# Performance work log

Hardware: AMD Instinct MI355X
Metric: run time of the kernel (lower is better)

Reference implementation:

```python
import jax, jax.numpy as jnp
import numpy as np

SCALE_BASE = 512.0
GAMMA = 0.96875


def _rotate_every_two(x):
    x1 = x[..., ::2]
    x2 = x[..., 1::2]
    return jnp.stack([-x2, x1], axis=-1).reshape(x.shape)


def _dup_interleave(m):
    # [L, d/2] -> [L, d], each column duplicated: (a,b) -> (a,a,b,b)
    return jnp.repeat(m, 2, axis=-1)


def _xpos(x, downscale=False):
    # x: [B, L, d]; offset = 0 (parallel form)
    B, L, d = x.shape
    half = d // 2
    pos = jnp.arange(L, dtype=x.dtype)
    # xpos per-channel scale base
    sv = (jnp.arange(0, d, 2, dtype=x.dtype) + 0.4 * d) / (1.4 * d)   # [d/2]
    scale = sv[None, :] ** (pos[:, None] / SCALE_BASE)                 # [L, d/2]
    if downscale:
        scale = 1.0 / scale
    inv_freq = 1.0 / (10000.0 ** (jnp.arange(half, dtype=x.dtype) / half))
    sinusoid = pos[:, None] * inv_freq[None, :]                        # [L, d/2]
    sin = _dup_interleave(jnp.sin(sinusoid) * scale)                   # [L, d]
    cos = _dup_interleave(jnp.cos(sinusoid) * scale)                   # [L, d]
    return x * cos[None] + _rotate_every_two(x) * sin[None]


def _get_D(seq_len, dtype):
    idx = jnp.arange(seq_len)
    diff = idx[:, None] - idx[None, :]                                 # n - m
    safe = jnp.where(diff >= 0, diff, 0).astype(dtype)
    return jnp.where(diff >= 0, GAMMA ** safe, jnp.zeros((), dtype))   # [L, L]


def setup_inputs() -> dict:
    key = jax.random.key(0)
    k1, k2, k3, k4 = jax.random.split(key, 4)
    B, L, H, D = 2, 4096, 1024, 64
    X = jax.random.normal(k1, (B, L, H), dtype=jnp.float32)
    W_Q = jax.random.normal(k2, (H, D), dtype=jnp.float32) / H
    W_K = jax.random.normal(k3, (H, D), dtype=jnp.float32) / H
    W_V = jax.random.normal(k4, (H, D), dtype=jnp.float32) / H
    return {"X": X, "W_Q": W_Q, "W_K": W_K, "W_V": W_V}


def reference(X, W_Q, W_K, W_V):
    L = X.shape[1]
    Dmask = _get_D(L, X.dtype)                     # [L, L]
    Q = _xpos(X @ W_Q)                             # [B, L, d]
    K = _xpos(X @ W_K, downscale=True)             # [B, L, d]
    V = X @ W_V                                    # [B, L, v]
    ret = jnp.einsum('bnd,bmd->bnm', Q, K) * Dmask[None]  # [B, L, L]
    return ret @ V                                 # [B, L, v]
```

## Files before the change

kernel.cpp:

```cpp
#include <hip/hip_runtime.h>
#include <math.h>

#define NB 2
#define LL 4096
#define HH 1024
#define DD 64
#define CHK 64
#define NCH 64
#define BLROWS (NB*LL)
#define NCHT (NB*NCH)
#define GAMMA 0.96875f

typedef _Float16 f16x8 __attribute__((ext_vector_type(8)));
typedef _Float16 f16x4 __attribute__((ext_vector_type(4)));
typedef float    f32x4 __attribute__((ext_vector_type(4)));

#define WCH 12288

__global__ __launch_bounds__(256) void prep_w(
    const float* __restrict__ WQ, const float* __restrict__ WK,
    const float* __restrict__ WV, _Float16* __restrict__ Whg,
    _Float16* __restrict__ Wlg)
{
    const unsigned t = blockIdx.x * 256 + threadIdx.x;
    const unsigned kchunk = t / 1536u;
    const unsigned s = t - kchunk * 1536u;
    const int ct2  = s >> 6;
    const int lane = s & 63;
    const int n16  = ct2 >> 1;
    const int kt   = ct2 & 1;
    const int quad = lane >> 4;
    const int n    = n16 * 16 + (lane & 15);
    const int k0   = (int)kchunk * 64 + kt * 32 + quad * 8;
    const int m    = n >> 6;
    const int d    = n & 63;
    const float* Wm = (m == 0) ? WQ : (m == 1) ? WK : WV;
    f16x8 hv, lv;
#pragma unroll
    for (int j = 0; j < 8; ++j) {
        const float x = Wm[(size_t)(k0 + j) * DD + d] * 1024.f;
        const _Float16 h = (_Float16)x;
        hv[j] = h;
        lv[j] = (_Float16)(x - (float)h);
    }
    *(f16x8*)&Whg[(size_t)t * 8] = hv;
    *(f16x8*)&Wlg[(size_t)t * 8] = lv;
}

__global__ __launch_bounds__(256) void proj_mfma(
    const float* __restrict__ X, const _Float16* __restrict__ Whg,
    const _Float16* __restrict__ Wlg, _Float16* __restrict__ Qr,
    _Float16* __restrict__ Kr, _Float16* __restrict__ Vr)
{
    __shared__ __align__(16) _Float16 lds[28672];
    _Float16* Xh = lds;
    _Float16* Xl = lds + 2048;
    _Float16* Wh = lds + 4096;
    _Float16* Wl = lds + 16384;

    const int tid  = threadIdx.x;
    const int wv   = tid >> 6;
    const int lane = tid & 63;
    const int r0   = blockIdx.x * 32;

    const int xrow = tid >> 3;
    const int xk8  = (tid & 7) * 8;
    const int xslot = (((xrow >> 4) * 2 + (xk8 >> 5)) * 64 +
                       ((xk8 >> 3) & 3) * 16 + (xrow & 15)) * 8;

    f32x4 acc[6];
#pragma unroll
    for (int i = 0; i < 6; ++i) acc[i] = (f32x4){0.f, 0.f, 0.f, 0.f};

    float4 pxa, pxb;
    f16x8  pwh[6], pwl[6];
    {
        const float* xp = &X[(size_t)(r0 + xrow) * HH + xk8];
        pxa = *(const float4*)&xp[0];
        pxb = *(const float4*)&xp[4];
#pragma unroll
        for (int i = 0; i < 6; ++i) {
            pwh[i] = *(const f16x8*)&Whg[(size_t)(tid + i * 256) * 8];
            pwl[i] = *(const f16x8*)&Wlg[(size_t)(tid + i * 256) * 8];
        }
    }

    for (int ch = 0; ch < 16; ++ch) {
        __syncthreads();
        {
            const float xv[8] = {pxa.x, pxa.y, pxa.z, pxa.w,
                                 pxb.x, pxb.y, pxb.z, pxb.w};
            f16x8 hv, lv;
#pragma unroll
            for (int e = 0; e < 8; ++e) {
                const _Float16 h = (_Float16)xv[e];
                hv[e] = h;
                lv[e] = (_Float16)(xv[e] - (float)h);
            }
            *(f16x8*)&Xh[xslot] = hv;
            *(f16x8*)&Xl[xslot] = lv;
#pragma unroll
            for (int i = 0; i < 6; ++i) {
                *(f16x8*)&Wh[(tid + i * 256) * 8] = pwh[i];
                *(f16x8*)&Wl[(tid + i * 256) * 8] = pwl[i];
            }
        }
        __syncthreads();
        if (ch + 1 < 16) {
            const float* xp = &X[(size_t)(r0 + xrow) * HH + (ch + 1) * 64 + xk8];
            pxa = *(const float4*)&xp[0];
            pxb = *(const float4*)&xp[4];
            const size_t cb = (size_t)(ch + 1) * WCH;
#pragma unroll
            for (int i = 0; i < 6; ++i) {
                pwh[i] = *(const f16x8*)&Whg[cb + (size_t)(tid + i * 256) * 8];
                pwl[i] = *(const f16x8*)&Wlg[cb + (size_t)(tid + i * 256) * 8];
            }
        }
#pragma unroll
        for (int kt = 0; kt < 2; ++kt) {
            const f16x8 a0h = *(const f16x8*)&Xh[((0 * 2 + kt) * 64 + lane) * 8];
            const f16x8 a0l = *(const f16x8*)&Xl[((0 * 2 + kt) * 64 + lane) * 8];
            const f16x8 a1h = *(const f16x8*)&Xh[((1 * 2 + kt) * 64 + lane) * 8];
            const f16x8 a1l = *(const f16x8*)&Xl[((1 * 2 + kt) * 64 + lane) * 8];
#pragma unroll
            for (int cj = 0; cj < 3; ++cj) {
                const int ctg = wv * 3 + cj;
                const f16x8 bh = *(const f16x8*)&Wh[((ctg * 2 + kt) * 64 + lane) * 8];
                const f16x8 bl = *(const f16x8*)&Wl[((ctg * 2 + kt) * 64 + lane) * 8];
                acc[cj] = __builtin_amdgcn_mfma_f32_16x16x32_f16(a0h, bh, acc[cj], 0, 0, 0);
                acc[cj] = __builtin_amdgcn_mfma_f32_16x16x32_f16(a0h, bl, acc[cj], 0, 0, 0);
                acc[cj] = __builtin_amdgcn_mfma_f32_16x16x32_f16(a0l, bh, acc[cj], 0, 0, 0);
                acc[3 + cj] = __builtin_amdgcn_mfma_f32_16x16x32_f16(a1h, bh, acc[3 + cj], 0, 0, 0);
                acc[3 + cj] = __builtin_amdgcn_mfma_f32_16x16x32_f16(a1h, bl, acc[3 + cj], 0, 0, 0);
                acc[3 + cj] = __builtin_amdgcn_mfma_f32_16x16x32_f16(a1l, bh, acc[3 + cj], 0, 0, 0);
            }
        }
    }

    const int quad = lane >> 4;
    const int c16  = lane & 15;
#pragma unroll
    for (int rt = 0; rt < 2; ++rt) {
#pragma unroll
        for (int cj = 0; cj < 3; ++cj) {
            const int ctg = wv * 3 + cj;
            const f32x4 v = acc[rt * 3 + cj];
            const int col = ctg * 16 + c16;
            const int mat = ctg >> 2;
            const int d   = col & 63;
            if (mat < 2) {
                const int i2 = d >> 1;
                const float sv   = (2.f * (float)i2 + 25.6f) / 89.6f;
                const float l2sv = log2f(sv);
                const float ifr  = exp2f(-13.28771237954945f * ((float)i2 / 32.f));
                const float sgn  = (mat == 0) ? 1.f : -1.f;
                _Float16* dst = (mat == 0) ? Qr : Kr;
#pragma unroll
                for (int r = 0; r < 4; ++r) {
                    const int row = r0 + rt * 16 + quad * 4 + r;
                    const float val = v[r] * (1.f / 1024.f);
                    const float p = __shfl_xor(val, 1, 64);
                    const float pf  = (float)(row & (LL - 1));
                    const float pfs = (float)(row & 63);
                    const float scl = exp2f(sgn * (pfs * (1.f / 512.f)) * l2sv);
                    float s, c;
                    sincosf(pf * ifr, &s, &c);
                    s *= scl; c *= scl;
                    const float o = ((col & 1) == 0) ? val * c - p * s
                                                     : val * c + p * s;
                    dst[(size_t)row * DD + d] = (_Float16)o;
                }
            } else {
#pragma unroll
                for (int r = 0; r < 4; ++r) {
                    const int row = r0 + rt * 16 + quad * 4 + r;
                    Vr[(size_t)row * DD + d] = (_Float16)(v[r] * (1.f / 1024.f));
                }
            }
        }
    }
}

__global__ __launch_bounds__(256) void chunk_kv(
    const _Float16* __restrict__ Kr, const _Float16* __restrict__ Vr,
    float* __restrict__ U)
{
    __shared__ _Float16 Kl[64 * 64];
    __shared__ _Float16 Vl[64 * 32];
    __shared__ float pwd[64];
    const int tid   = threadIdx.x;
    const int bc    = blockIdx.x;
    const int chunk = bc >> 1;
    const int dph   = (bc & 1) * 32;
    const size_t rbase = (size_t)chunk * CHK * DD;
    const float l2g = log2f(GAMMA);

    if (tid < 64) pwd[tid] = exp2f((float)(63 - tid) * l2g);
    {
        const int row = tid >> 2;
        const int c0  = (tid & 3) * 16;
        *(f16x8*)&Kl[row * 64 + c0]     = *(const f16x8*)&Kr[rbase + (size_t)row * DD + c0];
        *(f16x8*)&Kl[row * 64 + c0 + 8] = *(const f16x8*)&Kr[rbase + (size_t)row * DD + c0 + 8];
        const int c1 = (tid & 3) * 8;
        *(f16x8*)&Vl[row * 32 + c1] = *(const f16x8*)&Vr[rbase + (size_t)row * DD + dph + c1];
    }
    __syncthreads();
    const int dgr = tid >> 4;
    const int dc  = tid & 15;
    float a[4][2] = {{0,0},{0,0},{0,0},{0,0}};
#pragma unroll 8
    for (int j = 0; j < CHK; ++j) {
        const f16x4 kh = *(const f16x4*)&Kl[j * 64 + dgr * 4];
        const float w  = pwd[j];
        const float v0 = (float)Vl[j * 32 + dc * 2]     * w;
        const float v1 = (float)Vl[j * 32 + dc * 2 + 1] * w;
        const float k0 = (float)kh[0], k1 = (float)kh[1];
        const float k2 = (float)kh[2], k3 = (float)kh[3];
        a[0][0] += k0 * v0; a[0][1] += k0 * v1;
        a[1][0] += k1 * v0; a[1][1] += k1 * v1;
        a[2][0] += k2 * v0; a[2][1] += k2 * v1;
        a[3][0] += k3 * v0; a[3][1] += k3 * v1;
    }
#pragma unroll
    for (int r = 0; r < 4; ++r) {
        *(float2*)&U[((size_t)chunk * DD + dgr * 4 + r) * DD + dph + dc * 2] =
            make_float2(a[r][0], a[r][1]);
    }
}

__global__ __launch_bounds__(256) void prep_vt(
    const _Float16* __restrict__ Vr, const float* __restrict__ U,
    _Float16* __restrict__ VTf)
{
    __shared__ float    Tl[64 * 68];
    __shared__ _Float16 Vl[64 * 72];
    const int tid   = threadIdx.x;
    const int chunk = blockIdx.x;
    const int cloc  = chunk & 63;
    const size_t rbase = (size_t)chunk * CHK * DD;
    const float l2g = log2f(GAMMA);

    {
        const int row = tid >> 2;
        const int c0  = (tid & 3) * 16;
        *(f16x8*)&Vl[row * 72 + c0]     = *(const f16x8*)&Vr[rbase + (size_t)row * DD + c0];
        *(f16x8*)&Vl[row * 72 + c0 + 8] = *(const f16x8*)&Vr[rbase + (size_t)row * DD + c0 + 8];
    }
    {
        const int d  = tid >> 2;
        const int dq = (tid & 3) * 16;
        const float sv = (2.f * (float)(d >> 1) + 25.6f) / 89.6f;
        const float l2sv = log2f(sv);
        float acc[16];
#pragma unroll
        for (int i = 0; i < 16; ++i) acc[i] = 0.f;
        for (int dl = 1; dl <= 8; ++dl) {
            if (dl <= cloc) {
                const float f = exp2f(64.f * (float)(dl - 1) * l2g +
                                      0.125f * (float)dl * l2sv);
                const float* up = &U[((size_t)(chunk - dl) * DD + d) * DD + dq];
#pragma unroll
                for (int i4 = 0; i4 < 4; ++i4) {
                    const float4 u = *(const float4*)&up[i4 * 4];
                    acc[i4 * 4 + 0] += f * u.x; acc[i4 * 4 + 1] += f * u.y;
                    acc[i4 * 4 + 2] += f * u.z; acc[i4 * 4 + 3] += f * u.w;
                }
            }
        }
#pragma unroll
        for (int i = 0; i < 16; ++i) Tl[d * 68 + dq + i] = acc[i];
    }
    __syncthreads();
#pragma unroll
    for (int it = 0; it < 4; ++it) {
        const int s    = tid + it * 256;
        const int nt   = s >> 8;
        const int ks   = (s >> 6) & 3;
        const int lane = s & 63;
        const int quad = lane >> 4;
        const int dp   = nt * 16 + (lane & 15);
        const int mb   = ks * 32 + quad * 8;
        f16x8 v;
#pragma unroll
        for (int j = 0; j < 8; ++j) {
            const int mrow = mb + j;
            v[j] = (mrow < 64) ? Vl[mrow * 72 + dp]
                               : (_Float16)Tl[(mrow - 64) * 68 + dp];
        }
        *(f16x8*)&VTf[(size_t)chunk * 8192 + (size_t)s * 8] = v;
    }
}

__global__ __launch_bounds__(256) void chunk_out(
    const _Float16* __restrict__ Qr, const _Float16* __restrict__ Kr,
    const _Float16* __restrict__ VTf, float* __restrict__ out)
{
    __shared__ _Float16 Sb[32 * 136];
    __shared__ float pwl[65];
    const int tid   = threadIdx.x;
    const int bc    = blockIdx.x;
    const int chunk = bc >> 1;
    const int nh    = (bc & 1) * 32;
    const int w     = tid >> 6;
    const int lane  = tid & 63;
    const int quad  = lane >> 4;
    const int l15   = lane & 15;
    const int mtile = w >> 1;
    const int npair = (w & 1) * 2;
    const size_t rowbase = (size_t)chunk * CHK + nh;

    if (tid < 65) pwl[tid] = exp2f((float)tid * log2f(GAMMA));

    f16x8 aQ[2], bK[2][2];
#pragma unroll
    for (int ks = 0; ks < 2; ++ks)
        aQ[ks] = *(const f16x8*)&Qr[(rowbase + mtile * 16 + l15) * DD +
                                    ks * 32 + quad * 8];
#pragma unroll
    for (int nt = 0; nt < 2; ++nt)
#pragma unroll
        for (int ks = 0; ks < 2; ++ks)
            bK[nt][ks] = *(const f16x8*)&Kr[((size_t)chunk * CHK +
                                            (npair + nt) * 16 + l15) * DD +
                                            ks * 32 + quad * 8];
    __syncthreads();

    f32x4 sA[2] = {(f32x4){0.f,0.f,0.f,0.f}, (f32x4){0.f,0.f,0.f,0.f}};
#pragma unroll
    for (int nt = 0; nt < 2; ++nt)
#pragma unroll
        for (int ks = 0; ks < 2; ++ks)
            sA[nt] = __builtin_amdgcn_mfma_f32_16x16x32_f16(aQ[ks], bK[nt][ks],
                                                            sA[nt], 0, 0, 0);
#pragma unroll
    for (int nt = 0; nt < 2; ++nt) {
        const int m = (npair + nt) * 16 + l15;
#pragma unroll
        for (int r = 0; r < 4; ++r) {
            const int nl = mtile * 16 + quad * 4 + r;
            const int n64 = nh + nl;
            const float val = (n64 >= m) ? sA[nt][r] * pwl[n64 - m] : 0.f;
            Sb[nl * 136 + m] = (_Float16)val;
        }
    }
    if ((w & 1) == 0) {
        const float g = pwl[nh + mtile * 16 + l15 + 1];
#pragma unroll
        for (int ks = 0; ks < 2; ++ks) {
            f16x8 qv;
#pragma unroll
            for (int j = 0; j < 8; ++j)
                qv[j] = (_Float16)((float)aQ[ks][j] * g);
            *(f16x8*)&Sb[(mtile * 16 + l15) * 136 + 64 + ks * 32 + quad * 8] = qv;
        }
    }
    __syncthreads();

    f32x4 oA[2] = {(f32x4){0.f,0.f,0.f,0.f}, (f32x4){0.f,0.f,0.f,0.f}};
#pragma unroll
    for (int ks = 0; ks < 4; ++ks) {
        const f16x8 aS = *(const f16x8*)&Sb[(mtile * 16 + l15) * 136 +
                                            ks * 32 + quad * 8];
#pragma unroll
        for (int nt = 0; nt < 2; ++nt) {
            const f16x8 bV = *(const f16x8*)&VTf[(size_t)chunk * 8192 +
                (size_t)((((npair + nt) * 4 + ks) * 64 + lane)) * 8];
            oA[nt] = __builtin_amdgcn_mfma_f32_16x16x32_f16(aS, bV, oA[nt], 0, 0, 0);
        }
    }
#pragma unroll
    for (int nt = 0; nt < 2; ++nt)
#pragma unroll
        for (int r = 0; r < 4; ++r)
            out[(rowbase + mtile * 16 + quad * 4 + r) * DD +
                (npair + nt) * 16 + l15] = oA[nt][r];
}

extern "C" void kernel_launch(void* const* d_in, const int* in_sizes, int n_in,
                              void* d_out, int out_size, void* d_ws, size_t ws_size,
                              hipStream_t stream)
{
    const float* X  = (const float*)d_in[0];
    const float* WQ = (const float*)d_in[1];
    const float* WK = (const float*)d_in[2];
    const float* WV = (const float*)d_in[3];
    float* out = (float*)d_out;

    _Float16* Whg = (_Float16*)d_ws;
    _Float16* Wlg = Whg + 196608;
    _Float16* Qr  = Wlg + 196608;
    _Float16* Kr  = Qr + (size_t)BLROWS * DD;
    _Float16* Vr  = Kr + (size_t)BLROWS * DD;
    _Float16* VTf = Vr + (size_t)BLROWS * DD;
    float*    U   = (float*)(VTf + (size_t)NCHT * 8192);

    hipLaunchKernelGGL(prep_w, dim3(96), dim3(256), 0, stream,
                       WQ, WK, WV, Whg, Wlg);
    hipLaunchKernelGGL(proj_mfma, dim3(BLROWS / 32), dim3(256), 0, stream,
                       X, Whg, Wlg, Qr, Kr, Vr);
    hipLaunchKernelGGL(chunk_kv, dim3(2 * NCHT), dim3(256), 0, stream, Kr, Vr, U);
    hipLaunchKernelGGL(prep_vt, dim3(NCHT), dim3(256), 0, stream, Vr, U, VTf);
    hipLaunchKernelGGL(chunk_out, dim3(2 * NCHT), dim3(256), 0, stream,
                       Qr, Kr, VTf, out);
}
```

Before: 116.9 us.

## Drop LDS staging in projection and fuse prep_vt into chunk_out

The projection kernel now loads X fragments and the pre-split fp16 W hi/lo tiles straight from global memory into MFMA operand registers. This removes the LDS staging, the double-buffered prefetch and the per-chunk barriers. The separate prep_vt kernel is removed, and chunk_out now builds the V tile and the decayed inter-chunk state T in shared memory itself, then gathers the B operands from LDS. This saves one launch and the VTf round trip through global memory. In exchange, the T accumulation is done twice per chunk (once by each of the two half-chunk blocks), and W is read from global or L2 by every wave without reuse through LDS.

```diff
diff --git a/kernel.cpp b/kernel.cpp
--- a/kernel.cpp
+++ b/kernel.cpp
@@ -52,94 +52,63 @@
     const _Float16* __restrict__ Wlg, _Float16* __restrict__ Qr,
     _Float16* __restrict__ Kr, _Float16* __restrict__ Vr)
 {
-    __shared__ __align__(16) _Float16 lds[28672];
-    _Float16* Xh = lds;
-    _Float16* Xl = lds + 2048;
-    _Float16* Wh = lds + 4096;
-    _Float16* Wl = lds + 16384;
-
     const int tid  = threadIdx.x;
     const int wv   = tid >> 6;
     const int lane = tid & 63;
+    const int quad = lane >> 4;
+    const int l15  = lane & 15;
     const int r0   = blockIdx.x * 32;
 
-    const int xrow = tid >> 3;
-    const int xk8  = (tid & 7) * 8;
-    const int xslot = (((xrow >> 4) * 2 + (xk8 >> 5)) * 64 +
-                       ((xk8 >> 3) & 3) * 16 + (xrow & 15)) * 8;
-
     f32x4 acc[6];
 #pragma unroll
     for (int i = 0; i < 6; ++i) acc[i] = (f32x4){0.f, 0.f, 0.f, 0.f};
 
-    float4 pxa, pxb;
-    f16x8  pwh[6], pwl[6];
-    {
-        const float* xp = &X[(size_t)(r0 + xrow) * HH + xk8];
-        pxa = *(const float4*)&xp[0];
-        pxb = *(const float4*)&xp[4];
-#pragma unroll
-        for (int i = 0; i < 6; ++i) {
-            pwh[i] = *(const f16x8*)&Whg[(size_t)(tid + i * 256) * 8];
-            pwl[i] = *(const f16x8*)&Wlg[(size_t)(tid + i * 256) * 8];
-        }
-    }
-
     for (int ch = 0; ch < 16; ++ch) {
-        __syncthreads();
-        {
-            const float xv[8] = {pxa.x, pxa.y, pxa.z, pxa.w,
-                                 pxb.x, pxb.y, pxb.z, pxb.w};
-            f16x8 hv, lv;
-#pragma unroll
-            for (int e = 0; e < 8; ++e) {
-                const _Float16 h = (_Float16)xv[e];
-                hv[e] = h;
-                lv[e] = (_Float16)(xv[e] - (float)h);
-            }
-            *(f16x8*)&Xh[xslot] = hv;
-            *(f16x8*)&Xl[xslot] = lv;
-#pragma unroll
-            for (int i = 0; i < 6; ++i) {
-                *(f16x8*)&Wh[(tid + i * 256) * 8] = pwh[i];
-                *(f16x8*)&Wl[(tid + i * 256) * 8] = pwl[i];
-            }
-        }
-        __syncthreads();
-        if (ch + 1 < 16) {
-            const float* xp = &X[(size_t)(r0 + xrow) * HH + (ch + 1) * 64 + xk8];
-            pxa = *(const float4*)&xp[0];
-            pxb = *(const float4*)&xp[4];
-            const size_t cb = (size_t)(ch + 1) * WCH;
-#pragma unroll
-            for (int i = 0; i < 6; ++i) {
-                pwh[i] = *(const f16x8*)&Whg[cb + (size_t)(tid + i * 256) * 8];
-                pwl[i] = *(const f16x8*)&Wlg[cb + (size_t)(tid + i * 256) * 8];
+        f16x8 ah[2][2], al[2][2];
+#pragma unroll
+        for (int rt = 0; rt < 2; ++rt) {
+#pragma unroll
+            for (int kt = 0; kt < 2; ++kt) {
+                const float* xp = &X[(size_t)(r0 + rt * 16 + l15) * HH +
+                                     ch * 64 + kt * 32 + quad * 8];
+                const float4 xa = *(const float4*)&xp[0];
+                const float4 xb = *(const float4*)&xp[4];
+                const float xv[8] = {xa.x, xa.y, xa.z, xa.w,
+                                     xb.x, xb.y, xb.z, xb.w};
+                f16x8 hv, lv;
+#pragma unroll
+                for (int e = 0; e < 8; ++e) {
+                    const _Float16 h = (_Float16)xv[e];
+                    hv[e] = h;
+                    lv[e] = (_Float16)(xv[e] - (float)h);
+                }
+                ah[rt][kt] = hv;
+                al[rt][kt] = lv;
             }
         }
 #pragma unroll
         for (int kt = 0; kt < 2; ++kt) {
-            const f16x8 a0h = *(const f16x8*)&Xh[((0 * 2 + kt) * 64 + lane) * 8];
-            const f16x8 a0l = *(const f16x8*)&Xl[((0 * 2 + kt) * 64 + lane) * 8];
-            const f16x8 a1h = *(const f16x8*)&Xh[((1 * 2 + kt) * 64 + lane) * 8];
-            const f16x8 a1l = *(const f16x8*)&Xl[((1 * 2 + kt) * 64 + lane) * 8];
 #pragma unroll
             for (int cj = 0; cj < 3; ++cj) {
                 const int ctg = wv * 3 + cj;
-                const f16x8 bh = *(const f16x8*)&Wh[((ctg * 2 + kt) * 64 + lane) * 8];
-                const f16x8 bl = *(const f16x8*)&Wl[((ctg * 2 + kt) * 64 + lane) * 8];
-                acc[cj] = __builtin_amdgcn_mfma_f32_16x16x32_f16(a0h, bh, acc[cj], 0, 0, 0);
-                acc[cj] = __builtin_amdgcn_mfma_f32_16x16x32_f16(a0h, bl, acc[cj], 0, 0, 0);
-                acc[cj] = __builtin_amdgcn_mfma_f32_16x16x32_f16(a0l, bh, acc[cj], 0, 0, 0);
-                acc[3 + cj] = __builtin_amdgcn_mfma_f32_16x16x32_f16(a1h, bh, acc[3 + cj], 0, 0, 0);
-                acc[3 + cj] = __builtin_amdgcn_mfma_f32_16x16x32_f16(a1h, bl, acc[3 + cj], 0, 0, 0);
-                acc[3 + cj] = __builtin_amdgcn_mfma_f32_16x16x32_f16(a1l, bh, acc[3 + cj], 0, 0, 0);
-            }
-        }
-    }
-
-    const int quad = lane >> 4;
-    const int c16  = lane & 15;
+                const size_t off = (size_t)ch * WCH +
+                                   (size_t)(((ctg * 2 + kt) * 64 + lane)) * 8;
+                const f16x8 bh = *(const f16x8*)&Whg[off];
+                const f16x8 bl = *(const f16x8*)&Wlg[off];
+#pragma unroll
+                for (int rt = 0; rt < 2; ++rt) {
+                    acc[rt * 3 + cj] = __builtin_amdgcn_mfma_f32_16x16x32_f16(
+                        ah[rt][kt], bh, acc[rt * 3 + cj], 0, 0, 0);
+                    acc[rt * 3 + cj] = __builtin_amdgcn_mfma_f32_16x16x32_f16(
+                        ah[rt][kt], bl, acc[rt * 3 + cj], 0, 0, 0);
+                    acc[rt * 3 + cj] = __builtin_amdgcn_mfma_f32_16x16x32_f16(
+                        al[rt][kt], bh, acc[rt * 3 + cj], 0, 0, 0);
+                }
+            }
+        }
+    }
+
+    const int c16 = l15;
 #pragma unroll
     for (int rt = 0; rt < 2; ++rt) {
 #pragma unroll
@@ -229,75 +198,17 @@
     }
 }
 
-__global__ __launch_bounds__(256) void prep_vt(
-    const _Float16* __restrict__ Vr, const float* __restrict__ U,
-    _Float16* __restrict__ VTf)
-{
-    __shared__ float    Tl[64 * 68];
-    __shared__ _Float16 Vl[64 * 72];
-    const int tid   = threadIdx.x;
-    const int chunk = blockIdx.x;
-    const int cloc  = chunk & 63;
-    const size_t rbase = (size_t)chunk * CHK * DD;
-    const float l2g = log2f(GAMMA);
-
-    {
-        const int row = tid >> 2;
-        const int c0  = (tid & 3) * 16;
-        *(f16x8*)&Vl[row * 72 + c0]     = *(const f16x8*)&Vr[rbase + (size_t)row * DD + c0];
-        *(f16x8*)&Vl[row * 72 + c0 + 8] = *(const f16x8*)&Vr[rbase + (size_t)row * DD + c0 + 8];
-    }
-    {
-        const int d  = tid >> 2;
-        const int dq = (tid & 3) * 16;
-        const float sv = (2.f * (float)(d >> 1) + 25.6f) / 89.6f;
-        const float l2sv = log2f(sv);
-        float acc[16];
-#pragma unroll
-        for (int i = 0; i < 16; ++i) acc[i] = 0.f;
-        for (int dl = 1; dl <= 8; ++dl) {
-            if (dl <= cloc) {
-                const float f = exp2f(64.f * (float)(dl - 1) * l2g +
-                                      0.125f * (float)dl * l2sv);
-                const float* up = &U[((size_t)(chunk - dl) * DD + d) * DD + dq];
-#pragma unroll
-                for (int i4 = 0; i4 < 4; ++i4) {
-                    const float4 u = *(const float4*)&up[i4 * 4];
-                    acc[i4 * 4 + 0] += f * u.x; acc[i4 * 4 + 1] += f * u.y;
-                    acc[i4 * 4 + 2] += f * u.z; acc[i4 * 4 + 3] += f * u.w;
-                }
-            }
-        }
-#pragma unroll
-        for (int i = 0; i < 16; ++i) Tl[d * 68 + dq + i] = acc[i];
-    }
-    __syncthreads();
-#pragma unroll
-    for (int it = 0; it < 4; ++it) {
-        const int s    = tid + it * 256;
-        const int nt   = s >> 8;
-        const int ks   = (s >> 6) & 3;
-        const int lane = s & 63;
-        const int quad = lane >> 4;
-        const int dp   = nt * 16 + (lane & 15);
-        const int mb   = ks * 32 + quad * 8;
-        f16x8 v;
-#pragma unroll
-        for (int j = 0; j < 8; ++j) {
-            const int mrow = mb + j;
-            v[j] = (mrow < 64) ? Vl[mrow * 72 + dp]
-                               : (_Float16)Tl[(mrow - 64) * 68 + dp];
-        }
-        *(f16x8*)&VTf[(size_t)chunk * 8192 + (size_t)s * 8] = v;
-    }
-}
-
 __global__ __launch_bounds__(256) void chunk_out(
     const _Float16* __restrict__ Qr, const _Float16* __restrict__ Kr,
-    const _Float16* __restrict__ VTf, float* __restrict__ out)
-{
-    __shared__ _Float16 Sb[32 * 136];
-    __shared__ float pwl[65];
+    const _Float16* __restrict__ Vr, const float* __restrict__ U,
+    float* __restrict__ out)
+{
+    __shared__ __align__(16) unsigned char smraw[35648];
+    _Float16* Sb  = (_Float16*)smraw;
+    _Float16* Vl  = (_Float16*)(smraw + 8704);
+    float*    Tl  = (float*)(smraw + 17920);
+    float*    pwl = (float*)(smraw + 35328);
+
     const int tid   = threadIdx.x;
     const int bc    = blockIdx.x;
     const int chunk = bc >> 1;
@@ -309,8 +220,42 @@
     const int mtile = w >> 1;
     const int npair = (w & 1) * 2;
     const size_t rowbase = (size_t)chunk * CHK + nh;
-
-    if (tid < 65) pwl[tid] = exp2f((float)tid * log2f(GAMMA));
+    const float l2g = log2f(GAMMA);
+
+    if (tid < 65) pwl[tid] = exp2f((float)tid * l2g);
+
+    {
+        const int row = tid >> 2;
+        const int c0  = (tid & 3) * 16;
+        const size_t rb = (size_t)chunk * CHK * DD;
+        *(f16x8*)&Vl[row * 72 + c0]     = *(const f16x8*)&Vr[rb + (size_t)row * DD + c0];
+        *(f16x8*)&Vl[row * 72 + c0 + 8] = *(const f16x8*)&Vr[rb + (size_t)row * DD + c0 + 8];
+    }
+    {
+        const int d  = tid >> 2;
+        const int dq = (tid & 3) * 16;
+        const int cloc = chunk & 63;
+        const float sv = (2.f * (float)(d >> 1) + 25.6f) / 89.6f;
+        const float l2sv = log2f(sv);
+        float acc[16];
+#pragma unroll
+        for (int i = 0; i < 16; ++i) acc[i] = 0.f;
+        for (int dl = 1; dl <= 8; ++dl) {
+            if (dl <= cloc) {
+                const float f = exp2f(64.f * (float)(dl - 1) * l2g +
+                                      0.125f * (float)dl * l2sv);
+                const float* up = &U[((size_t)(chunk - dl) * DD + d) * DD + dq];
+#pragma unroll
+                for (int i4 = 0; i4 < 4; ++i4) {
+                    const float4 u = *(const float4*)&up[i4 * 4];
+                    acc[i4 * 4 + 0] += f * u.x; acc[i4 * 4 + 1] += f * u.y;
+                    acc[i4 * 4 + 2] += f * u.z; acc[i4 * 4 + 3] += f * u.w;
+                }
+            }
+        }
+#pragma unroll
+        for (int i = 0; i < 16; ++i) Tl[d * 68 + dq + i] = acc[i];
+    }
 
     f16x8 aQ[2], bK[2][2];
 #pragma unroll
@@ -364,8 +309,17 @@
                                             ks * 32 + quad * 8];
 #pragma unroll
         for (int nt = 0; nt < 2; ++nt) {
-            const f16x8 bV = *(const f16x8*)&VTf[(size_t)chunk * 8192 +
-                (size_t)((((npair + nt) * 4 + ks) * 64 + lane)) * 8];
+            const int dp = (npair + nt) * 16 + l15;
+            f16x8 bV;
+            if (ks < 2) {
+#pragma unroll
+                for (int j = 0; j < 8; ++j)
+                    bV[j] = Vl[(ks * 32 + quad * 8 + j) * 72 + dp];
+            } else {
+#pragma unroll
+                for (int j = 0; j < 8; ++j)
+                    bV[j] = (_Float16)Tl[((ks - 2) * 32 + quad * 8 + j) * 68 + dp];
+            }
             oA[nt] = __builtin_amdgcn_mfma_f32_16x16x32_f16(aS, bV, oA[nt], 0, 0, 0);
         }
     }
@@ -385,22 +339,20 @@
     const float* WQ = (const float*)d_in[1];
     const float* WK = (const float*)d_in[2];
     const float* WV = (const float*)d_in[3];
-    float* out = (float*)d_out;
+    float* outp = (float*)d_out;
 
     _Float16* Whg = (_Float16*)d_ws;
     _Float16* Wlg = Whg + 196608;
     _Float16* Qr  = Wlg + 196608;
     _Float16* Kr  = Qr + (size_t)BLROWS * DD;
     _Float16* Vr  = Kr + (size_t)BLROWS * DD;
-    _Float16* VTf = Vr + (size_t)BLROWS * DD;
-    float*    U   = (float*)(VTf + (size_t)NCHT * 8192);
+    float*    U   = (float*)(Vr + (size_t)BLROWS * DD);
 
     hipLaunchKernelGGL(prep_w, dim3(96), dim3(256), 0, stream,
                        WQ, WK, WV, Whg, Wlg);
     hipLaunchKernelGGL(proj_mfma, dim3(BLROWS / 32), dim3(256), 0, stream,
                        X, Whg, Wlg, Qr, Kr, Vr);
     hipLaunchKernelGGL(chunk_kv, dim3(2 * NCHT), dim3(256), 0, stream, Kr, Vr, U);
-    hipLaunchKernelGGL(prep_vt, dim3(NCHT), dim3(256), 0, stream, Vr, U, VTf);
     hipLaunchKernelGGL(chunk_out, dim3(2 * NCHT), dim3(256), 0, stream,
-                       Qr, Kr, VTf, out);
-}
+                       Qr, Kr, Vr, U, outp);
+}
```

Result: slower. 120.5 us (+3.1%).
